# Kernel optimization log

Measured on AMD Instinct MI355X. Metric: run time of the kernel, lower is better.

The kernel has to match this reference:

```python
import jax, jax.numpy as jnp
import numpy as np

HEADS = 20
SHIFT = 0.6931471805599453  # style_alignment_score_shift = log(2)
KEY_SCALE = 1.0             # style_alignment_score_scale
EPS = 1e-5


def expand_first(feat, scale=1.0):
    # feat: [B, H, S, D]; broadcast style features (batch items 0 and B//2)
    b = feat.shape[0]
    fs = jnp.stack([feat[0], feat[b // 2]])[:, None]           # [2,1,H,S,D]
    fs = jnp.broadcast_to(fs, (2, b // 2) + feat.shape[1:])    # [2,B/2,H,S,D]
    if scale != 1:
        fs = jnp.concatenate([fs[:, :1], scale * fs[:, 1:]], axis=1)
    return fs.reshape(feat.shape)


def concat_first(feat, scale=1.0):
    # concatenate style features along the sequence axis (-2)
    return jnp.concatenate([feat, expand_first(feat, scale=scale)], axis=-2)


def adain(feat):
    # stats over sequence axis (-2); torch .var() is unbiased (ddof=1)
    mean = feat.mean(axis=-2, keepdims=True)
    std = jnp.sqrt(feat.var(axis=-2, keepdims=True, ddof=1) + EPS)
    sm = expand_first(mean)
    ss = expand_first(std)
    return (feat - mean) / std * ss + sm


def setup_inputs() -> dict:
    key = jax.random.key(0)
    ks = jax.random.split(key, 6)
    B, S, C = 4, 1024, 1280
    sc = 1.0 / np.sqrt(C)
    return {
        "hidden_states": jax.random.normal(ks[0], (B, S, C), jnp.float32),
        "Wq": jax.random.normal(ks[1], (C, C), jnp.float32) * sc,
        "Wk": jax.random.normal(ks[2], (C, C), jnp.float32) * sc,
        "Wv": jax.random.normal(ks[3], (C, C), jnp.float32) * sc,
        "Wo": jax.random.normal(ks[4], (C, C), jnp.float32) * sc,
        "bo": jnp.zeros((C,), jnp.float32),
    }


def reference(hidden_states, Wq, Wk, Wv, Wo, bo):
    B, S, C = hidden_states.shape
    H = HEADS
    hd = C // H
    scale = hd ** -0.5

    def to_heads(t):  # [B,S,C] -> [B,H,S,hd]
        return t.reshape(B, S, H, hd).transpose(0, 2, 1, 3)

    q = to_heads(hidden_states @ Wq.T)
    k = to_heads(hidden_states @ Wk.T)
    v = to_heads(hidden_states @ Wv.T)

    q = adain(q)              # adain_queries
    k = adain(k)              # adain_keys
    # adain_values = False

    k = concat_first(k, scale=KEY_SCALE)   # [B,H,2S,hd]
    v = concat_first(v)                    # [B,H,2S,hd]

    # shifted scaled dot-product attention (shift added to shared-key block)
    logits = jnp.einsum('bhqd,bhkd->bhqk', q, k) * scale  # [B,H,S,2S]
    bias = jnp.where(jnp.arange(k.shape[-2]) >= S, jnp.float32(SHIFT), jnp.float32(0.0))
    probs = jax.nn.softmax(logits + bias, axis=-1)
    out = jnp.einsum('bhqk,bhkd->bhqd', probs, v)         # [B,H,S,hd]

    out = out.transpose(0, 2, 1, 3).reshape(B, S, C)
    out = out @ Wo.T + bo
    return out
```

## Files before the change

### kernel.cpp

```cpp
#include <hip/hip_runtime.h>
#include <math.h>


typedef __bf16 bf16x8 __attribute__((ext_vector_type(8)));
typedef __bf16 bf16x2_t __attribute__((ext_vector_type(2)));
typedef float f32x4 __attribute__((ext_vector_type(4)));
typedef unsigned short u16x8 __attribute__((ext_vector_type(8)));

#define BDIM 256

__device__ inline unsigned short f2bf(float f) {
  return __builtin_bit_cast(unsigned short, (__bf16)f);
}
__device__ inline unsigned int pack_bf2(float lo, float hi) {
  bf16x2_t v;
  v[0] = (__bf16)lo;
  v[1] = (__bf16)hi;
  return __builtin_bit_cast(unsigned int, v);
}
__device__ inline float bf2f(unsigned short h) {
  return __uint_as_float(((unsigned int)h) << 16);
}

__device__ inline void gl_lds16(const unsigned short* g, unsigned short* l) {
  __builtin_amdgcn_global_load_lds(
      (const __attribute__((address_space(1))) unsigned int*)g,
      (__attribute__((address_space(3))) unsigned int*)l, 16, 0, 0);
}

__global__ __launch_bounds__(BDIM) void k_convert_all(
    const float* __restrict__ X, const float* __restrict__ Wq,
    const float* __restrict__ Wk, const float* __restrict__ Wv,
    const float* __restrict__ Wo, unsigned short* __restrict__ Xbf,
    unsigned short* __restrict__ Wcat, unsigned short* __restrict__ Wobf) {
  const int idx = blockIdx.x * BDIM + threadIdx.x;
  const float* src;
  unsigned short* dst;
  int off;
  if (idx < 1310720) {
    src = X; dst = Xbf; off = idx;
  } else {
    const int r = idx - 1310720;
    const int which = r / 409600;
    off = r - which * 409600;
    src = (which == 0) ? Wq : (which == 1) ? Wk : (which == 2) ? Wv : Wo;
    dst = (which < 3) ? Wcat + (size_t)which * 1638400 : Wobf;
  }
  const float4 v = ((const float4*)src)[off];
  ushort4 o;
  o.x = f2bf(v.x); o.y = f2bf(v.y); o.z = f2bf(v.z); o.w = f2bf(v.w);
  ((ushort4*)dst)[off] = o;
}

__global__ __launch_bounds__(BDIM) void k_gemm_bf16(
    const unsigned short* __restrict__ A, const unsigned short* __restrict__ B,
    unsigned short* __restrict__ Cbf, int M, int N, int K) {
  __shared__ unsigned short As[2][128 * 32];
  __shared__ unsigned short Bs[2][128 * 32];
  const int t = threadIdx.x;
  const int w = t >> 6, lane = t & 63, quad = lane >> 4, l16 = lane & 15;
  const int wm = (w >> 1) << 6, wn = (w & 1) << 6;
  const int mBase = blockIdx.x * 128, nBase = blockIdx.y * 128;

  f32x4 acc[4][4];
#pragma unroll
  for (int i = 0; i < 4; i++)
#pragma unroll
    for (int j = 0; j < 4; j++) acc[i][j] = (f32x4){0.f, 0.f, 0.f, 0.f};

  const int r0 = t >> 2;
  const int kk0 = (t & 3) * 8;

  for (int k0 = 0; k0 < K; k0 += 64) {
    const unsigned short* Ab = A + (size_t)(mBase + r0) * K + k0 + kk0;
    const unsigned short* Bb = B + (size_t)(nBase + r0) * K + k0 + kk0;
    gl_lds16(Ab, As[0] + t * 8);
    gl_lds16(Ab + (size_t)64 * K, As[0] + (t + 256) * 8);
    gl_lds16(Ab + 32, As[1] + t * 8);
    gl_lds16(Ab + (size_t)64 * K + 32, As[1] + (t + 256) * 8);
    gl_lds16(Bb, Bs[0] + t * 8);
    gl_lds16(Bb + (size_t)64 * K, Bs[0] + (t + 256) * 8);
    gl_lds16(Bb + 32, Bs[1] + t * 8);
    gl_lds16(Bb + (size_t)64 * K + 32, Bs[1] + (t + 256) * 8);
    __syncthreads();
    bf16x8 af[2][4], bfr[2][4];
#pragma unroll
    for (int hh = 0; hh < 2; hh++)
#pragma unroll
      for (int i = 0; i < 4; i++) {
        af[hh][i] = *(const bf16x8*)(As[hh] + (wm + i * 16 + l16) * 32 + quad * 8);
        bfr[hh][i] = *(const bf16x8*)(Bs[hh] + (wn + i * 16 + l16) * 32 + quad * 8);
      }
#pragma unroll
    for (int hh = 0; hh < 2; hh++)
#pragma unroll
      for (int mi = 0; mi < 4; mi++)
#pragma unroll
        for (int ni = 0; ni < 4; ni++)
          acc[mi][ni] = __builtin_amdgcn_mfma_f32_16x16x32_bf16(
              af[hh][mi], bfr[hh][ni], acc[mi][ni], 0, 0, 0);
    __syncthreads();
  }

#pragma unroll
  for (int mi = 0; mi < 4; mi++)
#pragma unroll
    for (int r = 0; r < 4; r++) {
      const int row = mBase + wm + mi * 16 + quad * 4 + r;
#pragma unroll
      for (int ni = 0; ni < 4; ni++)
        Cbf[(size_t)row * N + nBase + wn + ni * 16 + l16] = f2bf(acc[mi][ni][r]);
    }
}

__global__ __launch_bounds__(BDIM) void k_gemm_64x128(
    const unsigned short* __restrict__ A, const unsigned short* __restrict__ B,
    float* __restrict__ Cf, const float* __restrict__ bias, int M, int N,
    int K) {
  __shared__ unsigned short As[2][64 * 32];
  __shared__ unsigned short Bs[2][128 * 32];
  const int t = threadIdx.x;
  const int w = t >> 6, lane = t & 63, quad = lane >> 4, l16 = lane & 15;
  const int wm = (w >> 1) << 5, wn = (w & 1) << 6;
  const int mBase = blockIdx.x * 64, nBase = blockIdx.y * 128;

  f32x4 acc[2][4];
#pragma unroll
  for (int i = 0; i < 2; i++)
#pragma unroll
    for (int j = 0; j < 4; j++) acc[i][j] = (f32x4){0.f, 0.f, 0.f, 0.f};

  const int r0 = t >> 2;
  const int kk0 = (t & 3) * 8;

  for (int k0 = 0; k0 < K; k0 += 64) {
    const unsigned short* Ab = A + (size_t)(mBase + r0) * K + k0 + kk0;
    const unsigned short* Bb = B + (size_t)(nBase + r0) * K + k0 + kk0;
    gl_lds16(Ab, As[0] + t * 8);
    gl_lds16(Ab + 32, As[1] + t * 8);
    gl_lds16(Bb, Bs[0] + t * 8);
    gl_lds16(Bb + (size_t)64 * K, Bs[0] + (t + 256) * 8);
    gl_lds16(Bb + 32, Bs[1] + t * 8);
    gl_lds16(Bb + (size_t)64 * K + 32, Bs[1] + (t + 256) * 8);
    __syncthreads();
    bf16x8 af[2][2], bfr[2][4];
#pragma unroll
    for (int hh = 0; hh < 2; hh++) {
#pragma unroll
      for (int i = 0; i < 2; i++)
        af[hh][i] = *(const bf16x8*)(As[hh] + (wm + i * 16 + l16) * 32 + quad * 8);
#pragma unroll
      for (int i = 0; i < 4; i++)
        bfr[hh][i] = *(const bf16x8*)(Bs[hh] + (wn + i * 16 + l16) * 32 + quad * 8);
    }
#pragma unroll
    for (int hh = 0; hh < 2; hh++)
#pragma unroll
      for (int mi = 0; mi < 2; mi++)
#pragma unroll
        for (int ni = 0; ni < 4; ni++)
          acc[mi][ni] = __builtin_amdgcn_mfma_f32_16x16x32_bf16(
              af[hh][mi], bfr[hh][ni], acc[mi][ni], 0, 0, 0);
    __syncthreads();
  }

#pragma unroll
  for (int mi = 0; mi < 2; mi++)
#pragma unroll
    for (int r = 0; r < 4; r++) {
      const int row = mBase + wm + mi * 16 + quad * 4 + r;
#pragma unroll
      for (int ni = 0; ni < 4; ni++) {
        const int col = nBase + wn + ni * 16 + l16;
        Cf[(size_t)row * N + col] = acc[mi][ni][r] + bias[col];
      }
    }
}

__global__ __launch_bounds__(320) void k_stats1(
    const unsigned short* __restrict__ QKV, float* __restrict__ psum,
    float* __restrict__ psq) {
  const int z = blockIdx.y, which = z >> 2, b = z & 3;
  const int c = threadIdx.x * 4;
  const size_t base =
      (size_t)(b * 1024 + blockIdx.x * 32) * 3840 + which * 1280 + c;
  float4 s = {0.f, 0.f, 0.f, 0.f}, s2 = {0.f, 0.f, 0.f, 0.f};
#pragma unroll 8
  for (int i = 0; i < 32; ++i) {
    const ushort4 xv = *(const ushort4*)(QKV + base + (size_t)i * 3840);
    const float x0 = bf2f(xv.x), x1 = bf2f(xv.y), x2 = bf2f(xv.z),
                x3 = bf2f(xv.w);
    s.x += x0; s.y += x1; s.z += x2; s.w += x3;
    s2.x = fmaf(x0, x0, s2.x); s2.y = fmaf(x1, x1, s2.y);
    s2.z = fmaf(x2, x2, s2.z); s2.w = fmaf(x3, x3, s2.w);
  }
  const size_t o = ((size_t)z * 32 + blockIdx.x) * 1280 + c;
  *(float4*)(psum + o) = s;
  *(float4*)(psq + o) = s2;
}

__global__ __launch_bounds__(BDIM) void k_stats2(
    const float* __restrict__ psum, const float* __restrict__ psq,
    float* __restrict__ stats) {
  const int z = blockIdx.y, which = z >> 2, b = z & 3;
  const int c = blockIdx.x * 256 + threadIdx.x;
  float s = 0.f, s2 = 0.f;
#pragma unroll
  for (int j = 0; j < 32; ++j) {
    s += psum[((size_t)z * 32 + j) * 1280 + c];
    s2 += psq[((size_t)z * 32 + j) * 1280 + c];
  }
  const float mean = s * (1.0f / 1024.0f);
  const float var = (s2 - 1024.0f * mean * mean) * (1.0f / 1023.0f);
  stats[((which * 2 + 0) * 4 + b) * 1280 + c] = mean;
  stats[((which * 2 + 1) * 4 + b) * 1280 + c] = sqrtf(var + 1e-5f);
}

__global__ __launch_bounds__(BDIM) void k_adain_vt(
    const unsigned short* __restrict__ QKV, const float* __restrict__ stats,
    unsigned short* __restrict__ qn, unsigned short* __restrict__ kn,
    unsigned short* __restrict__ vt) {
  __shared__ unsigned short tile[64][65];
  const int bx = blockIdx.x;
  if (bx < 10240) {
    const int which = bx / 5120;
    const int rem = bx - which * 5120;
    const int b = rem / 1280;
    const int xb = rem - b * 1280;
    const int idx = xb * BDIM + threadIdx.x;
    const int s = idx / 320;
    const int c = (idx - s * 320) * 4;
    const int sb = (b < 2) ? 0 : 2;
    const ushort4 xv = *(const ushort4*)(QKV + ((size_t)(b * 1024 + s)) * 3840 +
                                         which * 1280 + c);
    const float4 mean =
        *(const float4*)(stats + ((which * 2 + 0) * 4 + b) * 1280 + c);
    const float4 stdv =
        *(const float4*)(stats + ((which * 2 + 1) * 4 + b) * 1280 + c);
    const float4 meanS =
        *(const float4*)(stats + ((which * 2 + 0) * 4 + sb) * 1280 + c);
    const float4 stdS =
        *(const float4*)(stats + ((which * 2 + 1) * 4 + sb) * 1280 + c);
    ushort4 o;
    o.x = f2bf((bf2f(xv.x) - mean.x) / stdv.x * stdS.x + meanS.x);
    o.y = f2bf((bf2f(xv.y) - mean.y) / stdv.y * stdS.y + meanS.y);
    o.z = f2bf((bf2f(xv.z) - mean.z) / stdv.z * stdS.z + meanS.z);
    o.w = f2bf((bf2f(xv.w) - mean.w) / stdv.w * stdS.w + meanS.w);
    unsigned short* dst = (which == 0) ? qn : kn;
    *(ushort4*)(dst + ((size_t)(b * 1024 + s)) * 1280 + c) = o;
  } else {
    const int tb = bx - 10240;
    const int b = tb / 320;
    const int r2 = tb - b * 320;
    const int c0 = (r2 / 16) * 64;
    const int s0 = (r2 & 15) * 64;
    const int t = threadIdx.x;
    const int r = t >> 2, seg = (t & 3) * 16;
    const size_t goff = ((size_t)(b * 1024 + s0 + r)) * 3840 + 2560 + c0 + seg;
    const u16x8 va = *(const u16x8*)(QKV + goff);
    const u16x8 vb = *(const u16x8*)(QKV + goff + 8);
#pragma unroll
    for (int j = 0; j < 8; j++) {
      tile[r][seg + j] = va[j];
      tile[r][seg + 8 + j] = vb[j];
    }
    __syncthreads();
    u16x8 o0, o1;
#pragma unroll
    for (int j = 0; j < 8; j++) {
      o0[j] = tile[seg + j][r];
      o1[j] = tile[seg + 8 + j][r];
    }
    const size_t ooff = ((size_t)(b * 1280 + c0 + r)) * 1024 + s0 + seg;
    *(u16x8*)(vt + ooff) = o0;
    *(u16x8*)(vt + ooff + 8) = o1;
  }
}

__global__ __launch_bounds__(BDIM, 4) void k_attn(
    const unsigned short* __restrict__ qn, const unsigned short* __restrict__ kn,
    const unsigned short* __restrict__ vt, unsigned short* __restrict__ Opart,
    float* __restrict__ Lpart) {
  const int S = 1024, C = 1280;
  const int L = blockIdx.x + 8 * (blockIdx.y + 20 * blockIdx.z);
  const int qt = (L >> 3) & 7;
  const int hz = (L & 7) + ((L >> 6) << 3);
  const int h = hz % 20;
  const int zs = hz / 20;
  int b, chunk;
  if (zs < 2)      { b = 0; chunk = zs; }
  else if (zs < 6) { b = 1; chunk = zs - 2; }
  else if (zs < 8) { b = 2; chunk = zs - 6; }
  else             { b = 3; chunk = zs - 8; }
  const int ktBeg = chunk * 8;
  const int t = threadIdx.x, w = t >> 6, lane = t & 63;
  const int quad = lane >> 4, l16 = lane & 15;
  const int bstyle = (b < 2) ? 0 : 2;
  const int qrow = qt * 128 + w * 32;

  __shared__ unsigned short Ks[2][2][64 * 32];
  __shared__ unsigned short Vs[2][64 * 32];
  __shared__ unsigned short Plds[4][32][64];

  bf16x8 aq[2][2];
#pragma unroll
  for (int g = 0; g < 2; ++g) {
    const size_t qoff =
        ((size_t)(b * S + qrow + g * 16 + l16)) * C + h * 64 + quad * 8;
    aq[g][0] = *(const bf16x8*)(qn + qoff);
    aq[g][1] = *(const bf16x8*)(qn + qoff + 32);
  }

  bf16x8 ones;
#pragma unroll
  for (int i = 0; i < 8; ++i) ones[i] = (__bf16)1.0f;

  f32x4 o[2][4], lsum[2];
#pragma unroll
  for (int g = 0; g < 2; ++g) {
    lsum[g] = (f32x4){0.f, 0.f, 0.f, 0.f};
#pragma unroll
    for (int i = 0; i < 4; i++) o[g][i] = (f32x4){0.f, 0.f, 0.f, 0.f};
  }

  const int krow = t >> 2;
  const int kseg = (t & 3) * 8;
  const int sw = l16 & 14;

  auto stageK = [&](int buf, int kt) {
    const int bs = (kt < 16) ? b : bstyle;
    const int sk = (kt & 15) * 64;
    const unsigned short* kg =
        kn + (size_t)(bs * S + sk + krow) * C + h * 64 + kseg;
    gl_lds16(kg, Ks[buf][0] + t * 8);
    gl_lds16(kg + 32, Ks[buf][1] + t * 8);
  };
  auto stageV = [&](int kt) {
    const int bs = (kt < 16) ? b : bstyle;
    const int sk = (kt & 15) * 64;
    const unsigned short* vg =
        vt + (size_t)(bs * C + h * 64 + krow) * S + sk + kseg;
    gl_lds16(vg, Vs[0] + t * 8);
    gl_lds16(vg + 32, Vs[1] + t * 8);
  };

  stageK(0, ktBeg);

  const float SCALE2 = 0.125f * 1.44269504088896341f;

  for (int i = 0; i < 8; ++i) {
    const int kt = ktBeg + i;
    const int buf = i & 1;
    __syncthreads();
    stageV(kt);
    if (i + 1 < 8) stageK(buf ^ 1, kt + 1);

    const float bias2 = (kt >= 16) ? 1.0f : 0.0f;

    f32x4 z2[2][4];
#pragma unroll
    for (int nt = 0; nt < 4; ++nt) {
      const bf16x8 bk0 =
          *(const bf16x8*)(Ks[buf][0] + (nt * 16 + l16) * 32 + quad * 8);
      const bf16x8 bk1 =
          *(const bf16x8*)(Ks[buf][1] + (nt * 16 + l16) * 32 + quad * 8);
#pragma unroll
      for (int g = 0; g < 2; ++g) {
        f32x4 zz = (f32x4){0.f, 0.f, 0.f, 0.f};
        zz = __builtin_amdgcn_mfma_f32_16x16x32_bf16(bk0, aq[g][0], zz, 0, 0, 0);
        zz = __builtin_amdgcn_mfma_f32_16x16x32_bf16(bk1, aq[g][1], zz, 0, 0, 0);
        z2[g][nt] = zz;
      }
    }

#pragma unroll
    for (int g = 0; g < 2; ++g) {
#pragma unroll
      for (int nt = 0; nt < 4; ++nt) {
        const float e0 = exp2f(fmaf(z2[g][nt][0], SCALE2, bias2));
        const float e1 = exp2f(fmaf(z2[g][nt][1], SCALE2, bias2));
        const float e2 = exp2f(fmaf(z2[g][nt][2], SCALE2, bias2));
        const float e3 = exp2f(fmaf(z2[g][nt][3], SCALE2, bias2));
        uint2 pk;
        pk.x = pack_bf2(e0, e1);
        pk.y = pack_bf2(e2, e3);
        const int phys = (nt * 4 + quad) ^ sw;
        *(uint2*)(&Plds[w][g * 16 + l16][phys * 4]) = pk;
      }
    }

    __syncthreads();

#pragma unroll
    for (int g = 0; g < 2; ++g) {
      const int a0 = (2 * quad) ^ sw;
      const int a1 = (2 * quad + 8) ^ sw;
      const bf16x8 pa0 = *(const bf16x8*)(&Plds[w][g * 16 + l16][a0 * 4]);
      const bf16x8 pa1 = *(const bf16x8*)(&Plds[w][g * 16 + l16][a1 * 4]);
      lsum[g] = __builtin_amdgcn_mfma_f32_16x16x32_bf16(pa0, ones, lsum[g], 0, 0, 0);
      lsum[g] = __builtin_amdgcn_mfma_f32_16x16x32_bf16(pa1, ones, lsum[g], 0, 0, 0);
#pragma unroll
      for (int dt = 0; dt < 4; ++dt) {
        const bf16x8 vb0 =
            *(const bf16x8*)(Vs[0] + (dt * 16 + l16) * 32 + quad * 8);
        const bf16x8 vb1 =
            *(const bf16x8*)(Vs[1] + (dt * 16 + l16) * 32 + quad * 8);
        o[g][dt] =
            __builtin_amdgcn_mfma_f32_16x16x32_bf16(pa0, vb0, o[g][dt], 0, 0, 0);
        o[g][dt] =
            __builtin_amdgcn_mfma_f32_16x16x32_bf16(pa1, vb1, o[g][dt], 0, 0, 0);
      }
    }
  }

  if (l16 == 0) {
#pragma unroll
    for (int g = 0; g < 2; ++g)
#pragma unroll
      for (int r = 0; r < 4; ++r)
        Lpart[((size_t)zs * 20 + h) * 1024 + qrow + g * 16 + quad * 4 + r] =
            lsum[g][r];
  }

  unsigned short* Op = Opart + (size_t)zs * 1024 * 1280;
#pragma unroll
  for (int g = 0; g < 2; ++g)
#pragma unroll
    for (int dt = 0; dt < 4; ++dt)
#pragma unroll
      for (int r = 0; r < 4; ++r)
        Op[(size_t)(qrow + g * 16 + quad * 4 + r) * 1280 + h * 64 + dt * 16 +
           l16] = f2bf(o[g][dt][r]);
}

__global__ __launch_bounds__(BDIM) void k_combine(
    const unsigned short* __restrict__ Opart, const float* __restrict__ Lpart,
    unsigned short* __restrict__ attnb) {
  const int idx = blockIdx.x * BDIM + threadIdx.x;
  const int row = idx / 160;
  const int c = (idx - row * 160) * 8;
  const int b = row >> 10, q = row & 1023, h = c >> 6;
  const int zb = (b >> 1) * 6 + (b & 1) * 2;
  const int ns = 2 + (b & 1) * 2;
  float L = 0.f;
  float acc[8] = {0.f, 0.f, 0.f, 0.f, 0.f, 0.f, 0.f, 0.f};
  for (int s = 0; s < ns; ++s) {
    L += Lpart[((size_t)(zb + s) * 20 + h) * 1024 + q];
    const u16x8 v =
        *(const u16x8*)(Opart + (size_t)(zb + s) * 1310720 + (size_t)q * 1280 + c);
#pragma unroll
    for (int j = 0; j < 8; ++j) acc[j] += bf2f(v[j]);
  }
  const float rl = 1.0f / L;
  u16x8 o8;
#pragma unroll
  for (int j = 0; j < 8; ++j) o8[j] = f2bf(acc[j] * rl);
  *(u16x8*)(attnb + (size_t)row * 1280 + c) = o8;
}

extern "C" void kernel_launch(void* const* d_in, const int* in_sizes, int n_in,
                              void* d_out, int out_size, void* d_ws,
                              size_t ws_size, hipStream_t stream) {
  const float* X = (const float*)d_in[0];
  const float* Wq = (const float*)d_in[1];
  const float* Wk = (const float*)d_in[2];
  const float* Wv = (const float*)d_in[3];
  const float* Wo = (const float*)d_in[4];
  const float* bo = (const float*)d_in[5];
  float* out = (float*)d_out;

  char* ws = (char*)d_ws;
  size_t off = 0;
  auto alloc = [&](size_t bytes) {
    char* p = ws + off;
    off += (bytes + 255) & ~(size_t)255;
    return p;
  };
  unsigned short* Wcat = (unsigned short*)alloc(3840ull * 1280 * 2);
  unsigned short* Xbf = (unsigned short*)alloc(4096ull * 1280 * 2);
  unsigned short* QKV = (unsigned short*)alloc(4096ull * 3840 * 2);
  unsigned short* Wobf = (unsigned short*)alloc(1280ull * 1280 * 2);
  float* stats = (float*)alloc(2ull * 2 * 4 * 1280 * 4);
  unsigned short* qnb = (unsigned short*)alloc(4096ull * 1280 * 2);
  unsigned short* knb = (unsigned short*)alloc(4096ull * 1280 * 2);
  unsigned short* vtb = (unsigned short*)alloc(4096ull * 1280 * 2);
  unsigned short* attnb = (unsigned short*)alloc(4096ull * 1280 * 2);

  unsigned short* Opart = QKV;
  float* Lpart = (float*)Wcat;
  float* psum = (float*)attnb;
  float* psq = (float*)(attnb + 4096ull * 1280 / 2);

  k_convert_all<<<11520, BDIM, 0, stream>>>(X, Wq, Wk, Wv, Wo, Xbf, Wcat, Wobf);
  k_gemm_bf16<<<dim3(32, 30), BDIM, 0, stream>>>(Xbf, Wcat, QKV, 4096, 3840,
                                                 1280);
  k_stats1<<<dim3(32, 8), 320, 0, stream>>>(QKV, psum, psq);
  k_stats2<<<dim3(5, 8), BDIM, 0, stream>>>(psum, psq, stats);
  k_adain_vt<<<11520, BDIM, 0, stream>>>(QKV, stats, qnb, knb, vtb);
  k_attn<<<dim3(8, 20, 12), BDIM, 0, stream>>>(qnb, knb, vtb, Opart, Lpart);
  k_combine<<<2560, BDIM, 0, stream>>>(Opart, Lpart, attnb);
  k_gemm_64x128<<<dim3(64, 10), BDIM, 0, stream>>>(attnb, Wobf, out, bo, 4096,
                                                   1280, 1280);
}
```

Measured before the change: 273.4 us.

## Rewrite QKV GEMM with 256x256 tiles, swizzled LDS, double-buffered async staging

Replaces the 128x128 QKV projection GEMM with a 512-thread 256x256 tile kernel that XOR-swizzles LDS rows and overlaps the next k-tile's global-to-LDS loads with MFMA compute on the current tile. Blocks are remapped so consecutive block IDs spread across tiles, intended to improve L2 reuse, and setprio raises MFMA issue priority. The aim is more data reuse per loaded byte and fewer LDS bank conflicts. In exchange the kernel has high register pressure and only 240 blocks (about one wave on 256 CUs), and it relies on hand-placed vmcnt waits and barriers for correctness.

```diff
diff --git a/kernel.cpp b/kernel.cpp
--- a/kernel.cpp
+++ b/kernel.cpp
@@ -52,64 +52,101 @@
   ((ushort4*)dst)[off] = o;
 }
 
-__global__ __launch_bounds__(BDIM) void k_gemm_bf16(
+__global__ __launch_bounds__(512, 1) void k_gemm_bf16(
     const unsigned short* __restrict__ A, const unsigned short* __restrict__ B,
     unsigned short* __restrict__ Cbf, int M, int N, int K) {
-  __shared__ unsigned short As[2][128 * 32];
-  __shared__ unsigned short Bs[2][128 * 32];
+  __shared__ unsigned short lds[2][2][16384];
+
+  const int bid = blockIdx.x;
+  const int swz = (bid & 7) * 30 + (bid >> 3);
+  const int mt = swz & 15, nt = swz >> 4;
+  const int mBase = mt * 256, nBase = nt * 256;
+
   const int t = threadIdx.x;
   const int w = t >> 6, lane = t & 63, quad = lane >> 4, l16 = lane & 15;
-  const int wm = (w >> 1) << 6, wn = (w & 1) << 6;
-  const int mBase = blockIdx.x * 128, nBase = blockIdx.y * 128;
-
-  f32x4 acc[4][4];
-#pragma unroll
-  for (int i = 0; i < 4; i++)
-#pragma unroll
-    for (int j = 0; j < 4; j++) acc[i][j] = (f32x4){0.f, 0.f, 0.f, 0.f};
-
-  const int r0 = t >> 2;
-  const int kk0 = (t & 3) * 8;
-
-  for (int k0 = 0; k0 < K; k0 += 64) {
-    const unsigned short* Ab = A + (size_t)(mBase + r0) * K + k0 + kk0;
-    const unsigned short* Bb = B + (size_t)(nBase + r0) * K + k0 + kk0;
-    gl_lds16(Ab, As[0] + t * 8);
-    gl_lds16(Ab + (size_t)64 * K, As[0] + (t + 256) * 8);
-    gl_lds16(Ab + 32, As[1] + t * 8);
-    gl_lds16(Ab + (size_t)64 * K + 32, As[1] + (t + 256) * 8);
-    gl_lds16(Bb, Bs[0] + t * 8);
-    gl_lds16(Bb + (size_t)64 * K, Bs[0] + (t + 256) * 8);
-    gl_lds16(Bb + 32, Bs[1] + t * 8);
-    gl_lds16(Bb + (size_t)64 * K + 32, Bs[1] + (t + 256) * 8);
-    __syncthreads();
-    bf16x8 af[2][4], bfr[2][4];
-#pragma unroll
-    for (int hh = 0; hh < 2; hh++)
-#pragma unroll
-      for (int i = 0; i < 4; i++) {
-        af[hh][i] = *(const bf16x8*)(As[hh] + (wm + i * 16 + l16) * 32 + quad * 8);
-        bfr[hh][i] = *(const bf16x8*)(Bs[hh] + (wn + i * 16 + l16) * 32 + quad * 8);
+  const int wrow = w & 1, wcol = w >> 1;
+  const int glg = (lane & 7) ^ ((lane >> 3) & 7);
+  const int NTILES = K >> 6;
+
+  f32x4 acc[8][4];
+#pragma unroll
+  for (int i = 0; i < 8; ++i)
+#pragma unroll
+    for (int j = 0; j < 4; ++j) acc[i][j] = (f32x4){0.f, 0.f, 0.f, 0.f};
+
+  auto stage = [&](int s, int kt) {
+#pragma unroll
+    for (int j = 0; j < 4; ++j) {
+      const int row = j * 64 + w * 8 + (lane >> 3);
+      gl_lds16(A + (size_t)(mBase + row) * K + kt * 64 + glg * 8,
+               &lds[s][0][(j * 512 + w * 64 + lane) * 8]);
+    }
+#pragma unroll
+    for (int j = 0; j < 4; ++j) {
+      const int row = j * 64 + w * 8 + (lane >> 3);
+      gl_lds16(B + (size_t)(nBase + row) * K + kt * 64 + glg * 8,
+               &lds[s][1][(j * 512 + w * 64 + lane) * 8]);
+    }
+  };
+
+  stage(0, 0);
+  stage(1, 1);
+  asm volatile("s_waitcnt vmcnt(8)" ::: "memory");
+  __builtin_amdgcn_s_barrier();
+
+  const int arow0 = (wrow * 128 + l16) * 64;
+  const int brow0 = (wcol * 64 + l16) * 64;
+  const int g0 = ((quad) ^ (l16 & 7)) * 8;
+  const int g1 = ((4 + quad) ^ (l16 & 7)) * 8;
+
+  for (int kt = 0; kt < NTILES; ++kt) {
+    const int s = kt & 1;
+    if (kt >= 1 && kt + 1 < NTILES) stage(s ^ 1, kt + 1);
+    const unsigned short* As = &lds[s][0][0];
+    const unsigned short* Bs = &lds[s][1][0];
+#pragma unroll
+    for (int ph = 0; ph < 4; ++ph) {
+      const int mh = ph >> 1, nh = ph & 1;
+      bf16x8 af[4][2], bq[2][2];
+#pragma unroll
+      for (int mi = 0; mi < 4; ++mi) {
+        const int ro = arow0 + (mh * 4 + mi) * 1024;
+        af[mi][0] = *(const bf16x8*)(As + ro + g0);
+        af[mi][1] = *(const bf16x8*)(As + ro + g1);
       }
 #pragma unroll
-    for (int hh = 0; hh < 2; hh++)
-#pragma unroll
-      for (int mi = 0; mi < 4; mi++)
-#pragma unroll
-        for (int ni = 0; ni < 4; ni++)
-          acc[mi][ni] = __builtin_amdgcn_mfma_f32_16x16x32_bf16(
-              af[hh][mi], bfr[hh][ni], acc[mi][ni], 0, 0, 0);
-    __syncthreads();
-  }
-
-#pragma unroll
-  for (int mi = 0; mi < 4; mi++)
-#pragma unroll
-    for (int r = 0; r < 4; r++) {
-      const int row = mBase + wm + mi * 16 + quad * 4 + r;
-#pragma unroll
-      for (int ni = 0; ni < 4; ni++)
-        Cbf[(size_t)row * N + nBase + wn + ni * 16 + l16] = f2bf(acc[mi][ni][r]);
+      for (int ni = 0; ni < 2; ++ni) {
+        const int ro = brow0 + (nh * 2 + ni) * 1024;
+        bq[ni][0] = *(const bf16x8*)(Bs + ro + g0);
+        bq[ni][1] = *(const bf16x8*)(Bs + ro + g1);
+      }
+      __builtin_amdgcn_s_setprio(1);
+#pragma unroll
+      for (int kk = 0; kk < 2; ++kk)
+#pragma unroll
+        for (int mi = 0; mi < 4; ++mi)
+#pragma unroll
+          for (int ni = 0; ni < 2; ++ni)
+            acc[mh * 4 + mi][nh * 2 + ni] =
+                __builtin_amdgcn_mfma_f32_16x16x32_bf16(
+                    af[mi][kk], bq[ni][kk], acc[mh * 4 + mi][nh * 2 + ni], 0,
+                    0, 0);
+      __builtin_amdgcn_s_setprio(0);
+      if (ph < 3) __builtin_amdgcn_s_barrier();
+    }
+    asm volatile("s_waitcnt vmcnt(0)" ::: "memory");
+    __builtin_amdgcn_s_barrier();
+  }
+
+#pragma unroll
+  for (int mi = 0; mi < 8; ++mi)
+#pragma unroll
+    for (int r = 0; r < 4; ++r) {
+      const int row = mBase + wrow * 128 + mi * 16 + quad * 4 + r;
+#pragma unroll
+      for (int ni = 0; ni < 4; ++ni)
+        Cbf[(size_t)row * N + nBase + wcol * 64 + ni * 16 + l16] =
+            f2bf(acc[mi][ni][r]);
     }
 }
 
@@ -492,8 +529,7 @@
   float* psq = (float*)(attnb + 4096ull * 1280 / 2);
 
   k_convert_all<<<11520, BDIM, 0, stream>>>(X, Wq, Wk, Wv, Wo, Xbf, Wcat, Wobf);
-  k_gemm_bf16<<<dim3(32, 30), BDIM, 0, stream>>>(Xbf, Wcat, QKV, 4096, 3840,
-                                                 1280);
+  k_gemm_bf16<<<240, 512, 0, stream>>>(Xbf, Wcat, QKV, 4096, 3840, 1280);
   k_stats1<<<dim3(32, 8), 320, 0, stream>>>(QKV, psum, psq);
   k_stats2<<<dim3(5, 8), BDIM, 0, stream>>>(psum, psq, stats);
   k_adain_vt<<<11520, BDIM, 0, stream>>>(QKV, stats, qnb, knb, vtb);
```

New measurement: 263.4 us. 3.7% less time.
